# Optimization experiments

Hardware: AMD Instinct MI355X
Metric: run time of the kernel (lower is better)

## Reference

```python
import jax, jax.numpy as jnp
import numpy as np

B, CIN, H, W = 16, 32, 32, 32
OC, K = 64, 3
ALPHA = 0.0005625
VD = 0.1
DENOM = 2 * 1.5 * 0.025  # 2*n*VT
V_MIN, V_MAX = 0.0, 9.0
TH_MIN, TH_MAX = 1.0, 8.0


def setup_inputs() -> dict:
    key = jax.random.key(0)
    kx, kt = jax.random.split(key)
    x = jax.random.uniform(kx, (B, CIN, H, W), dtype=jnp.float32)
    # theta drawn in [TH_MIN, TH_MAX] so the in-forward clamp is an identity
    theta = jax.random.uniform(kt, (OC, CIN, K, K), dtype=jnp.float32,
                               minval=TH_MIN, maxval=TH_MAX)
    return {"x": x, "theta": theta}


def _ekv_f(v, t):
    # f(V, theta) = log(1 + exp(clip((V - theta)/denom, -50, 50)))**2
    arg = jnp.clip((v - t) / DENOM, -50.0, 50.0)
    return jnp.log1p(jnp.exp(arg)) ** 2


def reference(x, theta):
    theta_c = jnp.clip(theta, TH_MIN, TH_MAX)
    x_c = jnp.clip(x, V_MIN, V_MAX)
    # im2col: [B, CIN*K*K, Ho, Wo]; feature dim ordered (c, kh, kw) like torch unfold
    patches = jax.lax.conv_general_dilated_patches(
        x_c, filter_shape=(K, K), window_strides=(1, 1),
        padding=[(1, 1), (1, 1)])
    b, ckk, ho, wo = patches.shape
    vg = patches.reshape(b, ckk, ho * wo).transpose(0, 2, 1)  # [B, L, CKK]
    th = theta_c.reshape(OC, ckk)                              # [OC, CKK]
    # broadcast nonlinearity over output channels, reduce over patch dim
    vg4 = vg[:, :, None, :]          # [B, L, 1, CKK]
    th4 = th[None, None, :, :]       # [1, 1, OC, CKK]
    ik = ALPHA * jnp.sum(_ekv_f(vg4, th4) - _ekv_f(vg4, th4 + VD), axis=-1)  # [B, L, OC]
    return ik.transpose(0, 2, 1).reshape(b, OC, ho, wo)
```

## Files before the change

### kernel.cpp

```cpp
#include <hip/hip_runtime.h>


#define B_    16
#define CIN_  32
#define H_    32
#define W_    32
#define OC_   64
#define CKK_  288

#define INV_D  13.333333333333334f
#define ALPHA_ 0.0005625f
#define KC     0.26359713811572677f
#define C2_    0.93051654475128f
#define C3_    0.98168436111127f
#define C4_    0.91224137800000f

#define WS_VMAX   0
#define WS_CNTA   256
#define WS_CNTB   512
#define WS_LISTA  1024
#define WS_LISTB  (1024 + 64*288*8)
#define WS_NEEDED (WS_LISTB + 64*288*8)

__device__ __forceinline__ float clipf(float v, float lo, float hi) {
    return fminf(fmaxf(v, lo), hi);
}

__global__ void vmax_kernel(const float4* __restrict__ x4, unsigned* __restrict__ vmax, int n4) {
    float m = 0.0f;
    for (int i = blockIdx.x * blockDim.x + threadIdx.x; i < n4; i += gridDim.x * blockDim.x) {
        float4 v = x4[i];
        m = fmaxf(fmaxf(m, clipf(v.x, 0.0f, 9.0f)),
                  fmaxf(clipf(v.y, 0.0f, 9.0f),
                        fmaxf(clipf(v.z, 0.0f, 9.0f), clipf(v.w, 0.0f, 9.0f))));
    }
    #pragma unroll
    for (int off = 32; off > 0; off >>= 1)
        m = fmaxf(m, __shfl_down(m, off, 64));
    __shared__ float sm[4];
    int lane = threadIdx.x & 63, wid = threadIdx.x >> 6;
    if (lane == 0) sm[wid] = m;
    __syncthreads();
    if (threadIdx.x == 0) {
        float mm = fmaxf(fmaxf(sm[0], sm[1]), fmaxf(sm[2], sm[3]));
        atomicMax(vmax, __float_as_uint(mm));
    }
}

__global__ void build_lists(const float* __restrict__ theta,
                            const unsigned* __restrict__ vmax_u,
                            int* __restrict__ cntA, int* __restrict__ cntB,
                            int2* __restrict__ listA, int2* __restrict__ listB) {
    __shared__ int sA, sB;
    if (threadIdx.x == 0) { sA = 0; sB = 0; }
    __syncthreads();
    const int oc = blockIdx.x;
    const float vmax = __uint_as_float(*vmax_u);
    const float cutB = vmax + 0.6f;
    const float cutA = vmax + 0.131f;
    for (int j = threadIdx.x; j < CKK_; j += blockDim.x) {
        float t = clipf(theta[oc * CKK_ + j], 1.0f, 8.0f);
        if (t < cutB) {
            int cin = j / 9;
            int r   = j - cin * 9;
            int2 e;
            e.x = cin * 136 + (r / 3) * 34 + (r % 3);
            e.y = __float_as_int(__expf(-t * INV_D));
            if (t < cutA) { int i = atomicAdd(&sA, 1); listA[oc * CKK_ + i] = e; }
            else          { int i = atomicAdd(&sB, 1); listB[oc * CKK_ + i] = e; }
        }
    }
    __syncthreads();
    if (threadIdx.x == 0) { cntA[oc] = sA; cntB[oc] = sB; }
}

__launch_bounds__(256, 4)
__global__ void nlmain(const float* __restrict__ x,
                       const int* __restrict__ cntA, const int* __restrict__ cntB,
                       const int2* __restrict__ listA, const int2* __restrict__ listB,
                       float* __restrict__ out) {
    __shared__ float sx[CIN_ * 136];

    const int blk = blockIdx.x;
    const int ocg = blk & 3;
    const int rp  = (blk >> 2) & 15;
    const int b   = blk >> 6;

    for (int idx = threadIdx.x; idx < CIN_ * 136; idx += 256) {
        int cin = idx / 136;
        int rem = idx - cin * 136;
        int rr  = rem / 34;
        int cc  = rem - rr * 34;
        int ir  = rp * 2 - 1 + rr;
        int ic  = cc - 1;
        float ev = 1.0f;
        if ((unsigned)ir < (unsigned)H_ && (unsigned)ic < (unsigned)W_)
            ev = __expf(clipf(x[((b * CIN_ + cin) * H_ + ir) * W_ + ic], 0.0f, 9.0f) * INV_D);
        sx[idx] = ev;
    }
    __syncthreads();

    const int lane = threadIdx.x & 63;
    const int wv   = threadIdx.x >> 6;
    const int rl   = lane >> 5;
    const int w    = lane & 31;
    const int myoff = rl * 34 + w;
    const int row  = rp * 2 + rl;

    const int ocbase = __builtin_amdgcn_readfirstlane(ocg * 16 + wv * 4);

    #pragma unroll
    for (int k = 0; k < 4; ++k) {
        const int oc = ocbase + k;
        const int ca = cntA[oc];
        const int cb = cntB[oc];
        const int2* __restrict__ LA = listA + oc * CKK_;
        const int2* __restrict__ LB = listB + oc * CKK_;

        float accA = 0.0f, accB = 0.0f;

        #pragma unroll 2
        for (int i = 0; i < ca; ++i) {
            const int2 e  = LA[i];
            const float u = sx[e.x + myoff] * __int_as_float(e.y);
            const float l1 = __logf(1.0f + u);
            const float l2 = __logf(fmaf(u, KC, 1.0f));
            accA += (l1 - l2) * (l1 + l2);
        }
        #pragma unroll 4
        for (int i = 0; i < cb; ++i) {
            const int2 e  = LB[i];
            const float u = sx[e.x + myoff] * __int_as_float(e.y);
            float p = fmaf(u, C4_, -C3_);
            p = fmaf(u, p, C2_);
            accB = fmaf(u * u, p, accB);
        }

        out[((b * OC_ + oc) * H_ + row) * W_ + w] = ALPHA_ * (accA + accB);
    }
}

__launch_bounds__(256)
__global__ void nlconv_fallback(const float* __restrict__ x,
                                const float* __restrict__ theta,
                                float* __restrict__ out,
                                const unsigned* __restrict__ vmax_u) {
    __shared__ int   s_base[CKK_];
    __shared__ float s_t[CKK_];
    __shared__ int   s_d[CKK_];
    __shared__ int   s_cnt;
    const int blk = blockIdx.x;
    const int b  = blk >> 6;
    const int oc = blk & 63;
    if (threadIdx.x == 0) s_cnt = 0;
    __syncthreads();
    const float vmax   = __uint_as_float(*vmax_u);
    const float cutoff = vmax + 0.6f;
    for (int j = threadIdx.x; j < CKK_; j += blockDim.x) {
        float t = clipf(theta[oc * CKK_ + j], 1.0f, 8.0f);
        if (t < cutoff) {
            int i = atomicAdd(&s_cnt, 1);
            int cin = j / 9;
            int r   = j - cin * 9;
            s_base[i] = cin * (H_ * W_);
            s_t[i]    = t;
            s_d[i]    = (r / 3) | ((r % 3) << 8);
        }
    }
    __syncthreads();
    const int cnt = s_cnt;
    const float* xb = x + b * (CIN_ * H_ * W_);
    const int w  = threadIdx.x & 31;
    const int h0 = threadIdx.x >> 5;
    float acc[4] = {0.f, 0.f, 0.f, 0.f};
    for (int i = 0; i < cnt; ++i) {
        const float t    = s_t[i];
        const int   base = s_base[i];
        const int   d    = s_d[i];
        const int   rdh  = (d & 0xff) - 1;
        const int   rdw  = (d >> 8) - 1;
        const int  col   = w + rdw;
        const bool colok = (unsigned)col < (unsigned)W_;
        const int  ccol  = min(max(col, 0), W_ - 1);
        const float tq   = t * INV_D;
        #pragma unroll
        for (int k = 0; k < 4; ++k) {
            const int  row   = h0 + k * 8 + rdh;
            const bool rowok = (unsigned)row < (unsigned)H_;
            const int  crow  = min(max(row, 0), H_ - 1);
            const float xv   = xb[base + crow * W_ + ccol];
            const float v    = (rowok && colok) ? clipf(xv, 0.0f, 9.0f) : 0.0f;
            const float arg  = fmaf(v, INV_D, -tq);
            const float e1   = __expf(arg);
            const float e2   = e1 * KC;
            const float l1   = __logf(1.0f + e1);
            const float l2   = __logf(1.0f + e2);
            acc[k] += (l1 - l2) * (l1 + l2);
        }
    }
    float* ob = out + (b * OC_ + oc) * (H_ * W_);
    #pragma unroll
    for (int k = 0; k < 4; ++k)
        ob[(h0 + k * 8) * W_ + w] = ALPHA_ * acc[k];
}

extern "C" void kernel_launch(void* const* d_in, const int* in_sizes, int n_in,
                              void* d_out, int out_size, void* d_ws, size_t ws_size,
                              hipStream_t stream) {
    const float* x     = (const float*)d_in[0];
    const float* theta = (const float*)d_in[1];
    float* out = (float*)d_out;
    char* ws = (char*)d_ws;

    unsigned* vmax = (unsigned*)(ws + WS_VMAX);
    hipMemsetAsync(vmax, 0, sizeof(unsigned), stream);

    const int n4 = (B_ * CIN_ * H_ * W_) / 4;
    vmax_kernel<<<64, 256, 0, stream>>>((const float4*)x, vmax, n4);

    if (ws_size >= (size_t)WS_NEEDED) {
        int*  cntA  = (int*)(ws + WS_CNTA);
        int*  cntB  = (int*)(ws + WS_CNTB);
        int2* listA = (int2*)(ws + WS_LISTA);
        int2* listB = (int2*)(ws + WS_LISTB);

        build_lists<<<OC_, 128, 0, stream>>>(theta, vmax, cntA, cntB, listA, listB);
        nlmain<<<B_ * 16 * 4, 256, 0, stream>>>(x, cntA, cntB, listA, listB, out);
    } else {
        nlconv_fallback<<<B_ * OC_, 256, 0, stream>>>(x, theta, out, vmax);
    }
}
```

Measured before the change: 81.46 us.

## Replace atomic vmax memset with per-block partials; preload list entries into registers

The global atomicMax, which needed a preceding memset launch, is replaced by per-block partial maxima written to workspace, and each consumer reduces those 64 partials with a wave shuffle. This drops one stream operation. In the main kernel, each wave loads the first 64 list entries and the counts into registers before the shared-memory fill, so those global loads overlap with the exp staging. The inner loops then broadcast entries with readlane instead of loading per iteration, with a fallback loop for lists longer than 64. This raises register pressure, and readlane with a non-constant index may compile to a slower sequence.

```diff
diff --git a/kernel.cpp b/kernel.cpp
--- a/kernel.cpp
+++ b/kernel.cpp
@@ -15,7 +15,7 @@
 #define C3_    0.98168436111127f
 #define C4_    0.91224137800000f
 
-#define WS_VMAX   0
+#define WS_PART   0
 #define WS_CNTA   256
 #define WS_CNTB   512
 #define WS_LISTA  1024
@@ -26,7 +26,7 @@
     return fminf(fmaxf(v, lo), hi);
 }
 
-__global__ void vmax_kernel(const float4* __restrict__ x4, unsigned* __restrict__ vmax, int n4) {
+__global__ void vmax_part(const float4* __restrict__ x4, float* __restrict__ part, int n4) {
     float m = 0.0f;
     for (int i = blockIdx.x * blockDim.x + threadIdx.x; i < n4; i += gridDim.x * blockDim.x) {
         float4 v = x4[i];
@@ -41,21 +41,27 @@
     int lane = threadIdx.x & 63, wid = threadIdx.x >> 6;
     if (lane == 0) sm[wid] = m;
     __syncthreads();
-    if (threadIdx.x == 0) {
-        float mm = fmaxf(fmaxf(sm[0], sm[1]), fmaxf(sm[2], sm[3]));
-        atomicMax(vmax, __float_as_uint(mm));
-    }
+    if (threadIdx.x == 0)
+        part[blockIdx.x] = fmaxf(fmaxf(sm[0], sm[1]), fmaxf(sm[2], sm[3]));
+}
+
+__device__ __forceinline__ float reduce_vmax64(const float* __restrict__ part, int lane) {
+    float m = part[lane];
+    #pragma unroll
+    for (int off = 32; off > 0; off >>= 1)
+        m = fmaxf(m, __shfl_down(m, off, 64));
+    return __shfl(m, 0, 64);
 }
 
 __global__ void build_lists(const float* __restrict__ theta,
-                            const unsigned* __restrict__ vmax_u,
+                            const float* __restrict__ part,
                             int* __restrict__ cntA, int* __restrict__ cntB,
                             int2* __restrict__ listA, int2* __restrict__ listB) {
     __shared__ int sA, sB;
     if (threadIdx.x == 0) { sA = 0; sB = 0; }
+    const float vmax = reduce_vmax64(part, threadIdx.x & 63);
     __syncthreads();
     const int oc = blockIdx.x;
-    const float vmax = __uint_as_float(*vmax_u);
     const float cutB = vmax + 0.6f;
     const float cutA = vmax + 0.131f;
     for (int j = threadIdx.x; j < CKK_; j += blockDim.x) {
@@ -86,6 +92,21 @@
     const int rp  = (blk >> 2) & 15;
     const int b   = blk >> 6;
 
+    const int lane = threadIdx.x & 63;
+    const int wv   = threadIdx.x >> 6;
+    const int ocbase = ocg * 16 + wv * 4;
+
+    int  caV[4], cbV[4];
+    int2 eA[4], eB[4];
+    #pragma unroll
+    for (int k = 0; k < 4; ++k) {
+        const int oc = ocbase + k;
+        caV[k] = cntA[oc];
+        cbV[k] = cntB[oc];
+        eA[k]  = listA[oc * CKK_ + lane];
+        eB[k]  = listB[oc * CKK_ + lane];
+    }
+
     for (int idx = threadIdx.x; idx < CIN_ * 136; idx += 256) {
         int cin = idx / 136;
         int rem = idx - cin * 136;
@@ -100,36 +121,49 @@
     }
     __syncthreads();
 
-    const int lane = threadIdx.x & 63;
-    const int wv   = threadIdx.x >> 6;
-    const int rl   = lane >> 5;
-    const int w    = lane & 31;
+    const int rl    = lane >> 5;
+    const int w     = lane & 31;
     const int myoff = rl * 34 + w;
-    const int row  = rp * 2 + rl;
-
-    const int ocbase = __builtin_amdgcn_readfirstlane(ocg * 16 + wv * 4);
+    const int row   = rp * 2 + rl;
 
     #pragma unroll
     for (int k = 0; k < 4; ++k) {
         const int oc = ocbase + k;
-        const int ca = cntA[oc];
-        const int cb = cntB[oc];
-        const int2* __restrict__ LA = listA + oc * CKK_;
-        const int2* __restrict__ LB = listB + oc * CKK_;
+        const int ca = caV[k];
+        const int cb = cbV[k];
+        const int caR = min(ca, 64);
+        const int cbR = min(cb, 64);
 
         float accA = 0.0f, accB = 0.0f;
 
         #pragma unroll 2
-        for (int i = 0; i < ca; ++i) {
-            const int2 e  = LA[i];
-            const float u = sx[e.x + myoff] * __int_as_float(e.y);
+        for (int i = 0; i < caR; ++i) {
+            const int   off = __builtin_amdgcn_readlane(eA[k].x, i);
+            const float Et  = __int_as_float(__builtin_amdgcn_readlane(eA[k].y, i));
+            const float u   = sx[off + myoff] * Et;
+            const float l1  = __logf(1.0f + u);
+            const float l2  = __logf(fmaf(u, KC, 1.0f));
+            accA += (l1 - l2) * (l1 + l2);
+        }
+        #pragma unroll 4
+        for (int i = 0; i < cbR; ++i) {
+            const int   off = __builtin_amdgcn_readlane(eB[k].x, i);
+            const float Et  = __int_as_float(__builtin_amdgcn_readlane(eB[k].y, i));
+            const float u   = sx[off + myoff] * Et;
+            float p = fmaf(u, C4_, -C3_);
+            p = fmaf(u, p, C2_);
+            accB = fmaf(u * u, p, accB);
+        }
+
+        for (int i = 64; i < ca; ++i) {
+            const int2 e = listA[oc * CKK_ + i];
+            const float u  = sx[e.x + myoff] * __int_as_float(e.y);
             const float l1 = __logf(1.0f + u);
             const float l2 = __logf(fmaf(u, KC, 1.0f));
             accA += (l1 - l2) * (l1 + l2);
         }
-        #pragma unroll 4
-        for (int i = 0; i < cb; ++i) {
-            const int2 e  = LB[i];
+        for (int i = 64; i < cb; ++i) {
+            const int2 e = listB[oc * CKK_ + i];
             const float u = sx[e.x + myoff] * __int_as_float(e.y);
             float p = fmaf(u, C4_, -C3_);
             p = fmaf(u, p, C2_);
@@ -144,7 +178,7 @@
 __global__ void nlconv_fallback(const float* __restrict__ x,
                                 const float* __restrict__ theta,
                                 float* __restrict__ out,
-                                const unsigned* __restrict__ vmax_u) {
+                                const float* __restrict__ part) {
     __shared__ int   s_base[CKK_];
     __shared__ float s_t[CKK_];
     __shared__ int   s_d[CKK_];
@@ -153,8 +187,8 @@
     const int b  = blk >> 6;
     const int oc = blk & 63;
     if (threadIdx.x == 0) s_cnt = 0;
-    __syncthreads();
-    const float vmax   = __uint_as_float(*vmax_u);
+    const float vmax = reduce_vmax64(part, threadIdx.x & 63);
+    __syncthreads();
     const float cutoff = vmax + 0.6f;
     for (int j = threadIdx.x; j < CKK_; j += blockDim.x) {
         float t = clipf(theta[oc * CKK_ + j], 1.0f, 8.0f);
@@ -212,11 +246,10 @@
     float* out = (float*)d_out;
     char* ws = (char*)d_ws;
 
-    unsigned* vmax = (unsigned*)(ws + WS_VMAX);
-    hipMemsetAsync(vmax, 0, sizeof(unsigned), stream);
+    float* part = (float*)(ws + WS_PART);
 
     const int n4 = (B_ * CIN_ * H_ * W_) / 4;
-    vmax_kernel<<<64, 256, 0, stream>>>((const float4*)x, vmax, n4);
+    vmax_part<<<64, 256, 0, stream>>>((const float4*)x, part, n4);
 
     if (ws_size >= (size_t)WS_NEEDED) {
         int*  cntA  = (int*)(ws + WS_CNTA);
@@ -224,9 +257,9 @@
         int2* listA = (int2*)(ws + WS_LISTA);
         int2* listB = (int2*)(ws + WS_LISTB);
 
-        build_lists<<<OC_, 128, 0, stream>>>(theta, vmax, cntA, cntB, listA, listB);
+        build_lists<<<OC_, 128, 0, stream>>>(theta, part, cntA, cntB, listA, listB);
         nlmain<<<B_ * 16 * 4, 256, 0, stream>>>(x, cntA, cntB, listA, listB, out);
     } else {
-        nlconv_fallback<<<B_ * OC_, 256, 0, stream>>>(x, theta, out, vmax);
-    }
-}
+        nlconv_fallback<<<B_ * OC_, 256, 0, stream>>>(x, theta, out, part);
+    }
+}
```

Result: slower. 86.68 us (+6.4%).
